# Optimization experiments

Measured on AMD Instinct MI355X. Metric: run time of the kernel, lower is better.

## Reference

```python
import jax, jax.numpy as jnp
import numpy as np

# irreps: 4096x0e + 4096x1o + 4096x2e + 4096x3o (in == out)
MULS = [4096, 4096, 4096, 4096]
DIMS = [1, 3, 5, 7]  # 2l+1 for l = 0,1,2,3

def _build_paths():
    paths = []
    off = 0
    w_ptr = 0
    for mul, d in zip(MULS, DIMS):
        # (input offset, mul_in, ir dim, weight offset, mul_out)
        paths.append((off, mul, d, w_ptr, mul))
        off += mul * d
        w_ptr += mul * mul
    return paths

PATHS = _build_paths()
DIM_TOT = sum(m * d for m, d in zip(MULS, DIMS))  # 65536
W_TOT = sum(m * m for m in MULS)                  # 67108864


def setup_inputs() -> dict:
    key = jax.random.key(0)
    k1, k2 = jax.random.split(key)
    inp = jax.random.normal(k1, (DIM_TOT,), dtype=jnp.float32)
    weights = jax.random.normal(k2, (W_TOT,), dtype=jnp.float32)
    return {"input": inp, "weights": weights}


def reference(input, weights):
    chunks = []
    for off, mul_in, d, w_off, mul_out in PATHS:
        chunk_in = input[off:off + mul_in * d].reshape(mul_in, d)
        w = weights[w_off:w_off + mul_in * mul_out].reshape(mul_in, mul_out)
        norm = np.float32(np.sqrt(1.0 / mul_in))
        # 'ui,uv->vi' then ravel: output is (mul_out, d) flattened
        chunk_out = jnp.einsum('ui,uv->vi', chunk_in, w).reshape(-1) * norm
        chunks.append(chunk_out)
    return jnp.concatenate(chunks)
```

## Files before the change

### kernel.cpp

```cpp
#include <hip/hip_runtime.h>
#include <stdint.h>


constexpr int MUL = 4096;
constexpr int VT  = 64;
constexpr int NQ  = 16;
constexpr int SC  = 4;
constexpr int SCU = MUL / SC;
constexpr int UPT = SCU / NQ;
constexpr int PF  = 16;

template<int D>
__device__ __forceinline__ void body(
    const float* __restrict__ w, const float* __restrict__ x,
    float* __restrict__ out, float* xs, float* red,
    int io_off, long w_off, int v0)
{
  const int t  = threadIdx.x;
  const int lv = t & 63;
  const int q  = t >> 6;
  const long wcol = w_off + v0 + lv;

  float acc[D];
  #pragma unroll
  for (int i = 0; i < D; ++i) acc[i] = 0.f;

  for (int c = 0; c < SC; ++c) {
    const int ub = c * SCU;
    __syncthreads();
    for (int j = t; j < SCU * D; j += 1024)
      xs[j] = x[io_off + ub * D + j];
    __syncthreads();

    const int u0 = q * UPT;
    for (int bb = 0; bb < UPT; bb += PF) {
      float wv[PF];
      #pragma unroll
      for (int j = 0; j < PF; ++j)
        wv[j] = w[wcol + (long)(ub + u0 + bb + j) * MUL];
      #pragma unroll
      for (int j = 0; j < PF; ++j) {
        const float* xr = xs + (u0 + bb + j) * D;
        #pragma unroll
        for (int i = 0; i < D; ++i)
          acc[i] = fmaf(wv[j], xr[i], acc[i]);
      }
    }
  }

  #pragma unroll
  for (int i = 0; i < D; ++i)
    red[q * VT * D + lv * D + i] = acc[i];
  __syncthreads();

  for (int j = t; j < VT * D; j += 1024) {
    float s = 0.f;
    #pragma unroll
    for (int qq = 0; qq < NQ; ++qq) s += red[qq * VT * D + j];
    out[io_off + v0 * D + j] = s * 0.015625f;
  }
}

__global__ __launch_bounds__(1024)
void linear_all(const float* __restrict__ w, const float* __restrict__ x,
                float* __restrict__ out)
{
  __shared__ float xs [SCU * 7];
  __shared__ float red[NQ * VT * 7];
  const int b  = blockIdx.x;
  const int p  = b >> 6;
  const int v0 = (b & 63) * VT;

  if      (p == 0) body<1>(w, x, out, xs, red,     0,         0L, v0);
  else if (p == 1) body<3>(w, x, out, xs, red,  4096, 16777216L, v0);
  else if (p == 2) body<5>(w, x, out, xs, red, 16384, 33554432L, v0);
  else             body<7>(w, x, out, xs, red, 36864, 50331648L, v0);
}

extern "C" void kernel_launch(void* const* d_in, const int* in_sizes, int n_in,
                              void* d_out, int out_size, void* d_ws, size_t ws_size,
                              hipStream_t stream) {
  const float* x = (const float*)d_in[0];
  const float* w = (const float*)d_in[1];
  linear_all<<<256, 1024, 0, stream>>>(w, x, (float*)d_out);
}
```

Baseline: 361.5 us.

## Split reduction dimension across blocks with float4 weight loads and atomic accumulation

```diff
diff --git a/kernel.cpp b/kernel.cpp
--- a/kernel.cpp
+++ b/kernel.cpp
@@ -3,78 +3,111 @@
 
 
 constexpr int MUL = 4096;
-constexpr int VT  = 64;
-constexpr int NQ  = 16;
-constexpr int SC  = 4;
-constexpr int SCU = MUL / SC;
-constexpr int UPT = SCU / NQ;
-constexpr int PF  = 16;
+constexpr int VT  = 256;
+constexpr int NW  = 16;
+constexpr int UCB = 1024;
+constexpr int UPW = UCB / NW;
+constexpr int PF  = 8;
+constexpr int LDSF = 8 * 64 * 29;
+
+__global__ __launch_bounds__(256)
+void zero_out(float* __restrict__ out) {
+  out[blockIdx.x * 256 + threadIdx.x] = 0.f;
+}
 
 template<int D>
-__device__ __forceinline__ void body(
-    const float* __restrict__ w, const float* __restrict__ x,
-    float* __restrict__ out, float* xs, float* red,
-    int io_off, long w_off, int v0)
+__device__ __forceinline__ void body(const float* __restrict__ w,
+                                     const float* __restrict__ x,
+                                     float* __restrict__ out,
+                                     float* lds,
+                                     int io_off, long w_off, int v0, int u_base)
 {
-  const int t  = threadIdx.x;
-  const int lv = t & 63;
-  const int q  = t >> 6;
-  const long wcol = w_off + v0 + lv;
+  const int t = threadIdx.x;
+  const int l = t & 63;
+  const int q = t >> 6;
 
-  float acc[D];
+  float* xs = lds;
+  for (int j = t; j < UCB * D; j += 1024)
+    xs[j] = x[io_off + u_base * D + j];
+  __syncthreads();
+
+  float acc[D][4];
   #pragma unroll
-  for (int i = 0; i < D; ++i) acc[i] = 0.f;
+  for (int i = 0; i < D; ++i) {
+    #pragma unroll
+    for (int j = 0; j < 4; ++j) acc[i][j] = 0.f;
+  }
 
-  for (int c = 0; c < SC; ++c) {
-    const int ub = c * SCU;
-    __syncthreads();
-    for (int j = t; j < SCU * D; j += 1024)
-      xs[j] = x[io_off + ub * D + j];
-    __syncthreads();
+  const float* wp = w + w_off + (long)(u_base + q * UPW) * MUL + v0 + l * 4;
 
-    const int u0 = q * UPT;
-    for (int bb = 0; bb < UPT; bb += PF) {
-      float wv[PF];
+  for (int bb = 0; bb < UPW; bb += PF) {
+    float4 wv[PF];
+    #pragma unroll
+    for (int j = 0; j < PF; ++j)
+      wv[j] = *reinterpret_cast<const float4*>(wp + (long)(bb + j) * MUL);
+    #pragma unroll
+    for (int j = 0; j < PF; ++j) {
+      const float* xr = xs + (q * UPW + bb + j) * D;
       #pragma unroll
-      for (int j = 0; j < PF; ++j)
-        wv[j] = w[wcol + (long)(ub + u0 + bb + j) * MUL];
-      #pragma unroll
-      for (int j = 0; j < PF; ++j) {
-        const float* xr = xs + (u0 + bb + j) * D;
-        #pragma unroll
-        for (int i = 0; i < D; ++i)
-          acc[i] = fmaf(wv[j], xr[i], acc[i]);
+      for (int i = 0; i < D; ++i) {
+        float xv = xr[i];
+        acc[i][0] = fmaf(wv[j].x, xv, acc[i][0]);
+        acc[i][1] = fmaf(wv[j].y, xv, acc[i][1]);
+        acc[i][2] = fmaf(wv[j].z, xv, acc[i][2]);
+        acc[i][3] = fmaf(wv[j].w, xv, acc[i][3]);
       }
     }
   }
 
-  #pragma unroll
-  for (int i = 0; i < D; ++i)
-    red[q * VT * D + lv * D + i] = acc[i];
-  __syncthreads();
+  constexpr int SLAB = 4 * D + 1;
+  float* red = lds;
+  for (int step = NW / 2; step >= 1; step >>= 1) {
+    __syncthreads();
+    if (q >= step && q < 2 * step) {
+      float* rp = red + ((q - step) * 64 + l) * SLAB;
+      #pragma unroll
+      for (int j = 0; j < 4; ++j) {
+        #pragma unroll
+        for (int i = 0; i < D; ++i) rp[j * D + i] = acc[i][j];
+      }
+    }
+    __syncthreads();
+    if (q < step) {
+      const float* rp = red + (q * 64 + l) * SLAB;
+      #pragma unroll
+      for (int j = 0; j < 4; ++j) {
+        #pragma unroll
+        for (int i = 0; i < D; ++i) acc[i][j] += rp[j * D + i];
+      }
+    }
+  }
 
-  for (int j = t; j < VT * D; j += 1024) {
-    float s = 0.f;
+  if (q == 0) {
+    float* op = out + io_off + (size_t)(v0 + l * 4) * D;
     #pragma unroll
-    for (int qq = 0; qq < NQ; ++qq) s += red[qq * VT * D + j];
-    out[io_off + v0 * D + j] = s * 0.015625f;
+    for (int j = 0; j < 4; ++j) {
+      #pragma unroll
+      for (int i = 0; i < D; ++i)
+        atomicAdd(&op[j * D + i], acc[i][j] * 0.015625f);
+    }
   }
 }
 
 __global__ __launch_bounds__(1024)
-void linear_all(const float* __restrict__ w, const float* __restrict__ x,
-                float* __restrict__ out)
+void linear_main(const float* __restrict__ w, const float* __restrict__ x,
+                 float* __restrict__ out)
 {
-  __shared__ float xs [SCU * 7];
-  __shared__ float red[NQ * VT * 7];
+  __shared__ float lds[LDSF];
   const int b  = blockIdx.x;
   const int p  = b >> 6;
-  const int v0 = (b & 63) * VT;
+  const int r  = b & 63;
+  const int v0 = (r >> 2) * VT;
+  const int ub = (r & 3) * UCB;
 
-  if      (p == 0) body<1>(w, x, out, xs, red,     0,         0L, v0);
-  else if (p == 1) body<3>(w, x, out, xs, red,  4096, 16777216L, v0);
-  else if (p == 2) body<5>(w, x, out, xs, red, 16384, 33554432L, v0);
-  else             body<7>(w, x, out, xs, red, 36864, 50331648L, v0);
+  if      (p == 0) body<1>(w, x, out, lds,     0,         0L, v0, ub);
+  else if (p == 1) body<3>(w, x, out, lds,  4096, 16777216L, v0, ub);
+  else if (p == 2) body<5>(w, x, out, lds, 16384, 33554432L, v0, ub);
+  else             body<7>(w, x, out, lds, 36864, 50331648L, v0, ub);
 }
 
 extern "C" void kernel_launch(void* const* d_in, const int* in_sizes, int n_in,
@@ -82,5 +115,8 @@
                               hipStream_t stream) {
   const float* x = (const float*)d_in[0];
   const float* w = (const float*)d_in[1];
-  linear_all<<<256, 1024, 0, stream>>>(w, x, (float*)d_out);
+  float* out = (float*)d_out;
+
+  zero_out<<<256, 256, 0, stream>>>(out);
+  linear_main<<<256, 1024, 0, stream>>>(w, x, out);
 }
```

Result: no change. 365.2 us (+1.0%).
